# Kernel tuning notes

Hardware: AMD Instinct MI355X
Metric: run time of the kernel (lower is better)

## Reference

```python
import jax, jax.numpy as jnp
import numpy as np


def _unpack_int4(w_i32):
    # w_i32: [N, K//8] int32, 8 signed int4 nibbles per int32 (low nibble first)
    shifts = jnp.arange(8, dtype=jnp.int32) * 4
    nib = (w_i32[:, :, None] >> shifts[None, None, :]) & 0xF  # [N, K//8, 8]
    signed = (nib ^ 8) - 8  # map [0,15] -> [-8,7]
    N = w_i32.shape[0]
    return signed.reshape(N, -1)  # [N, K] int32 in [-8,7]


def setup_inputs() -> dict:
    key = jax.random.key(0)
    k1, k2, k3, k4, k5 = jax.random.split(key, 5)
    M, K, N, G = 4096, 4096, 14336, 128
    qx = jax.random.normal(k1, (M, K), dtype=jnp.float32)
    qxscale = jax.random.uniform(k2, (M, 1), dtype=jnp.float32, minval=0.5, maxval=1.5)
    weight_i4 = jax.random.randint(k3, (N, K // 8), 0, 2147483647, dtype=jnp.int32)
    weight_scale = jax.random.uniform(k4, (N, K // G), dtype=jnp.float32, minval=0.001, maxval=0.02)
    bias = jax.random.normal(k5, (N,), dtype=jnp.float32) * 0.02
    return {"qx": qx, "qxscale": qxscale, "weight_i4": weight_i4,
            "weight_scale": weight_scale, "bias": bias, "group_size": G}


def reference(qx, qxscale, weight_i4, weight_scale, bias, group_size):
    # 1) unpack int32 -> int4  2) per-group dequant  3) matmul  4) scale+bias  5) silu
    iweight = _unpack_int4(weight_i4)  # [N, K]
    N, K = iweight.shape
    deq_w = (iweight.astype(jnp.float32).reshape(N, K // group_size, group_size)
             * weight_scale[:, :, None]).reshape(N, K)  # [N, K]
    y = jnp.einsum('mk,nk->mn', qx, deq_w) * qxscale  # [M, N]
    y = y + bias[None, :]
    return jax.nn.silu(y)
```

## Files before the change

kernel.cpp:

```cpp
#include <hip/hip_runtime.h>
#include <hip/hip_bf16.h>
#include <stdint.h>


#define M_DIM 4096
#define K_DIM 4096
#define N_DIM 14336
#define GSZ   128

typedef __bf16 bf16x8 __attribute__((ext_vector_type(8)));
typedef __bf16 bf16x4 __attribute__((ext_vector_type(4)));
typedef float  f32x4  __attribute__((ext_vector_type(4)));
typedef float  f32x16 __attribute__((ext_vector_type(16)));

#define GLOAD16(g, l) __builtin_amdgcn_global_load_lds( \
    (const __attribute__((address_space(1))) void*)(g), \
    (__attribute__((address_space(3))) void*)(l), 16, 0, 0)

#define WAITVM(N) asm volatile("s_waitcnt vmcnt(" #N ")" ::: "memory")
#define WAITLGKM0() asm volatile("s_waitcnt lgkmcnt(0)" ::: "memory")


__global__ __launch_bounds__(256) void convertA_kernel(
    const float* __restrict__ qx, __bf16* __restrict__ out)
{
    const size_t i = ((size_t)blockIdx.x * 256 + threadIdx.x) * 8;
    const float4 a = *(const float4*)(qx + i);
    const float4 b = *(const float4*)(qx + i + 4);
    bf16x8 v;
    v[0] = (__bf16)a.x; v[1] = (__bf16)a.y; v[2] = (__bf16)a.z; v[3] = (__bf16)a.w;
    v[4] = (__bf16)b.x; v[5] = (__bf16)b.y; v[6] = (__bf16)b.z; v[7] = (__bf16)b.w;
    *(bf16x8*)(out + i) = v;
}

__global__ __launch_bounds__(256) void dequantW_kernel(
    const int* __restrict__ wq, const float* __restrict__ wscale,
    __bf16* __restrict__ out)
{
    const size_t g = (size_t)blockIdx.x * 256 + threadIdx.x;
    const int n  = (int)(g >> 9);
    const int wi = (int)(g & 511);
    const float s = wscale[(size_t)n * (K_DIM / GSZ) + (wi >> 4)];
    const int w = wq[g];
    bf16x8 v;
    #pragma unroll
    for (int j = 0; j < 8; ++j) {
        const int q = ((int)((unsigned)w << (28 - 4 * j))) >> 28;
        v[j] = (__bf16)((float)q * s);
    }
    *(bf16x8*)(out + g * 8) = v;
}


constexpr int BM = 256, BN = 256, BK = 64;
constexpr int NT  = K_DIM / BK;
constexpr int NIT = NT / 2;
constexpr int BUF_BYTES = 65536;

__global__ __launch_bounds__(512, 2) void gemm256_kernel(
    const __bf16* __restrict__ A,
    const __bf16* __restrict__ B,
    const float* __restrict__ qxscale,
    const float* __restrict__ bias,
    float* __restrict__ out)
{
    __shared__ __align__(16) char smem[2 * BUF_BYTES];

    const int t    = threadIdx.x;
    const int lane = t & 63;
    const int wave = t >> 6;
    const int wr   = wave >> 2;
    const int wc   = wave & 3;

    const int bid = blockIdx.x;
    const int cpx = (M_DIM / BM) * (N_DIM / BN) / 8;
    const int wg  = (bid & 7) * cpx + (bid >> 3);
    const int tiles_n = N_DIM / BN;
    const int tm = wg / tiles_n, tn = wg % tiles_n;
    const int m0 = tm * BM, n0 = tn * BN;

    const int srow = t >> 3;
    const int sg16 = (((t & 7) ^ (srow & 7)) << 4);
    const size_t KB = (size_t)K_DIM * 2;
    const char* aS = (const char*)A + (size_t)(m0 + srow) * KB + sg16;
    const char* bS = (const char*)B + (size_t)(n0 + srow) * KB + sg16;
    char* sbase = smem;

    auto STAGE_AQ = [&](int tile, int q) {
        GLOAD16(aS + (size_t)tile * 128 + (size_t)q * 64 * KB,
                sbase + (tile & 1) * BUF_BYTES + q * 8192 + t * 16);
    };
    auto STAGE_BQ = [&](int tile, int q) {
        GLOAD16(bS + (size_t)tile * 128 + (size_t)q * 64 * KB,
                sbase + (tile & 1) * BUF_BYTES + 32768 + q * 8192 + t * 16);
    };

    const int lane31 = lane & 31;
    const int h      = lane >> 5;
    const int swz0   = ((h ^ (lane31 & 7)) << 4);
    const int aB = (wr * 128 + lane31) * 128 + swz0;
    const int bB = 32768 + (wc * 64 + lane31) * 128 + swz0;

    f32x16 acc[4][2] = {};
    bf16x8 af[2][4], bfr[2][4];

    auto DS_A = [&](const char* buf, int mibase) {
        #pragma unroll
        for (int mi = 0; mi < 2; ++mi)
            #pragma unroll
            for (int kk = 0; kk < 4; ++kk)
                af[mi][kk] = *(const bf16x8*)(buf +
                    ((aB + (mibase + mi) * 4096) ^ (kk << 5)));
    };
    auto DS_B = [&](const char* buf, int ni) {
        #pragma unroll
        for (int kk = 0; kk < 4; ++kk)
            bfr[ni][kk] = *(const bf16x8*)(buf +
                ((bB + ni * 4096) ^ (kk << 5)));
    };
    auto MQ = [&](int mib, int ni) {
        #pragma unroll
        for (int kk = 0; kk < 4; ++kk)
            #pragma unroll
            for (int mi = 0; mi < 2; ++mi)
                acc[mib + mi][ni] = __builtin_amdgcn_mfma_f32_32x32x16_bf16(
                    af[mi][kk], bfr[ni][kk], acc[mib + mi][ni], 0, 0, 0);
    };

    #define PH_SYNC() do { __builtin_amdgcn_s_barrier(); WAITLGKM0(); \
        __builtin_amdgcn_sched_barrier(0); __builtin_amdgcn_s_setprio(1); } while (0)
    #define PH_END() do { __builtin_amdgcn_s_setprio(0); \
        __builtin_amdgcn_s_barrier(); } while (0)

    #pragma unroll
    for (int q = 0; q < 4; ++q) STAGE_AQ(0, q);
    #pragma unroll
    for (int q = 0; q < 4; ++q) STAGE_BQ(0, q);
    STAGE_AQ(1, 0); STAGE_AQ(1, 2);
    #pragma unroll
    for (int q = 0; q < 4; ++q) STAGE_BQ(1, q);
    WAITVM(6);
    __builtin_amdgcn_s_barrier();
    __builtin_amdgcn_sched_barrier(0);

    for (int i = 0; i < NIT; ++i) {
        const int t0 = 2 * i, t1 = 2 * i + 1;
        const bool more = (i + 1 < NIT);
        const char* bufE = sbase;
        const char* bufO = sbase + BUF_BYTES;

        DS_A(bufE, 0); DS_B(bufE, 0);
        STAGE_AQ(t1, 1); STAGE_AQ(t1, 3);
        PH_SYNC(); MQ(0, 0); PH_END();

        DS_B(bufE, 1);
        if (more) { STAGE_AQ(t0 + 2, 0); STAGE_AQ(t0 + 2, 2); }
        PH_SYNC(); MQ(0, 1); PH_END();

        DS_A(bufE, 2);
        if (more) { STAGE_BQ(t0 + 2, 0); STAGE_BQ(t0 + 2, 1); }
        PH_SYNC(); MQ(2, 1); PH_END();

        if (more) { STAGE_BQ(t0 + 2, 2); STAGE_BQ(t0 + 2, 3); WAITVM(6); }
        else      { WAITVM(0); }
        __builtin_amdgcn_s_barrier();
        __builtin_amdgcn_sched_barrier(0);
        __builtin_amdgcn_s_setprio(1);
        MQ(2, 0);
        PH_END();

        DS_A(bufO, 0); DS_B(bufO, 0);
        if (more) { STAGE_AQ(t0 + 2, 1); STAGE_AQ(t0 + 2, 3); }
        PH_SYNC(); MQ(0, 0); PH_END();

        DS_B(bufO, 1);
        if (more) { STAGE_AQ(t1 + 2, 0); STAGE_AQ(t1 + 2, 2); }
        PH_SYNC(); MQ(0, 1); PH_END();

        DS_A(bufO, 2);
        if (more) { STAGE_BQ(t1 + 2, 0); STAGE_BQ(t1 + 2, 1); }
        PH_SYNC(); MQ(2, 1); PH_END();

        if (more) { STAGE_BQ(t1 + 2, 2); STAGE_BQ(t1 + 2, 3); WAITVM(6); }
        __builtin_amdgcn_s_barrier();
        __builtin_amdgcn_sched_barrier(0);
        __builtin_amdgcn_s_setprio(1);
        MQ(2, 0);
        PH_END();
    }

    #undef PH_SYNC
    #undef PH_END

    const int c_col = lane31;
    const int hh4   = h * 4;
    float bv[2];
    #pragma unroll
    for (int ni = 0; ni < 2; ++ni)
        bv[ni] = bias[n0 + wc * 64 + ni * 32 + c_col];
    #pragma unroll
    for (int mi = 0; mi < 4; ++mi) {
        #pragma unroll
        for (int rq = 0; rq < 4; ++rq) {
            const int mg = m0 + wr * 128 + mi * 32 + rq * 8 + hh4;
            float qs[4];
            #pragma unroll
            for (int r = 0; r < 4; ++r) qs[r] = qxscale[mg + r];
            #pragma unroll
            for (int ni = 0; ni < 2; ++ni) {
                const int ng = n0 + wc * 64 + ni * 32 + c_col;
                #pragma unroll
                for (int r = 0; r < 4; ++r) {
                    const float y = acc[mi][ni][rq * 4 + r] * qs[r] + bv[ni];
                    out[(size_t)(mg + r) * N_DIM + ng] = y / (1.f + __expf(-y));
                }
            }
        }
    }
}


constexpr int FBM = 128, FBN = 128, FBK = 64;
constexpr int FLDA = 72;

__global__ __launch_bounds__(256) void gateproj_fused_kernel(
    const float* __restrict__ qx, const float* __restrict__ qxscale,
    const int* __restrict__ wq, const float* __restrict__ wscale,
    const float* __restrict__ bias, float* __restrict__ out)
{
    __shared__ __bf16 sA[FBM * FLDA];
    __shared__ __bf16 sB[FBN * FLDA];

    const int tid  = threadIdx.x;
    const int lane = tid & 63;
    const int wave = tid >> 6;
    const int wm = wave >> 1, wn = wave & 1;

    const int bid = blockIdx.x;
    const int cpx = (M_DIM / FBM) * (N_DIM / FBN) / 8;
    const int wg  = (bid & 7) * cpx + (bid >> 3);
    const int tiles_n = N_DIM / FBN;
    const int tm = wg / tiles_n, tn = wg % tiles_n;
    const int m0 = tm * FBM, n0 = tn * FBN;

    const int a_row = tid >> 4;
    const int a_col = (tid & 15) * 4;
    const float* aPtr = qx + (size_t)(m0 + a_row) * K_DIM + a_col;

    const int b_row = tid >> 1;
    const int b_wb  = (tid & 1) * 4;
    const int*   bPtr = wq     + (size_t)(n0 + b_row) * (K_DIM / 8) + b_wb;
    const float* sPtr = wscale + (size_t)(n0 + b_row) * (K_DIM / GSZ);

    float4 aReg[8];
    int    bRegW[4];
    float  bScl;
    f32x4 acc[4][4] = {};

    auto LOAD = [&](int kt) {
        const float* ap = aPtr + kt * FBK;
        #pragma unroll
        for (int i = 0; i < 8; ++i)
            aReg[i] = *(const float4*)(ap + (size_t)i * 16 * K_DIM);
        int4 b = *(const int4*)(bPtr + kt * 8);
        bRegW[0] = b.x; bRegW[1] = b.y; bRegW[2] = b.z; bRegW[3] = b.w;
        bScl = sPtr[kt >> 1];
    };

    auto STORE = [&]() {
        #pragma unroll
        for (int i = 0; i < 8; ++i) {
            bf16x4 v;
            v[0] = (__bf16)aReg[i].x; v[1] = (__bf16)aReg[i].y;
            v[2] = (__bf16)aReg[i].z; v[3] = (__bf16)aReg[i].w;
            *(bf16x4*)&sA[(a_row + i * 16) * FLDA + a_col] = v;
        }
        const int cb = (tid & 1) * 32;
        #pragma unroll
        for (int wi = 0; wi < 4; ++wi) {
            const int w = bRegW[wi];
            bf16x8 o;
            #pragma unroll
            for (int j = 0; j < 8; ++j) {
                const int v = ((int)((unsigned)w << (28 - 4 * j))) >> 28;
                o[j] = (__bf16)((float)v * bScl);
            }
            *(bf16x8*)&sB[b_row * FLDA + cb + wi * 8] = o;
        }
    };

    LOAD(0); STORE(); __syncthreads();

    const int FNT = K_DIM / FBK;
    for (int kt = 0; kt < FNT; ++kt) {
        if (kt + 1 < FNT) LOAD(kt + 1);
        #pragma unroll
        for (int kk = 0; kk < 2; ++kk) {
            bf16x8 af2[4], bfr2[4];
            const int ko = kk * 32 + (lane >> 4) * 8;
            #pragma unroll
            for (int mi = 0; mi < 4; ++mi)
                af2[mi] = *(const bf16x8*)&sA[(wm * 64 + mi * 16 + (lane & 15)) * FLDA + ko];
            #pragma unroll
            for (int ni = 0; ni < 4; ++ni)
                bfr2[ni] = *(const bf16x8*)&sB[(wn * 64 + ni * 16 + (lane & 15)) * FLDA + ko];
            #pragma unroll
            for (int mi = 0; mi < 4; ++mi)
                #pragma unroll
                for (int ni = 0; ni < 4; ++ni)
                    acc[mi][ni] = __builtin_amdgcn_mfma_f32_16x16x32_bf16(
                        af2[mi], bfr2[ni], acc[mi][ni], 0, 0, 0);
        }
        __syncthreads();
        if (kt + 1 < FNT) { STORE(); __syncthreads(); }
    }

    const int c_col = lane & 15;
    const int c_r4  = (lane >> 4) * 4;
    #pragma unroll
    for (int mi = 0; mi < 4; ++mi) {
        const int mg = m0 + wm * 64 + mi * 16 + c_r4;
        float qs[4];
        #pragma unroll
        for (int r = 0; r < 4; ++r) qs[r] = qxscale[mg + r];
        #pragma unroll
        for (int ni = 0; ni < 4; ++ni) {
            const int ng = n0 + wn * 64 + ni * 16 + c_col;
            const float bv = bias[ng];
            #pragma unroll
            for (int r = 0; r < 4; ++r) {
                const float y = acc[mi][ni][r] * qs[r] + bv;
                out[(size_t)(mg + r) * N_DIM + ng] = y / (1.f + __expf(-y));
            }
        }
    }
}


extern "C" void kernel_launch(void* const* d_in, const int* in_sizes, int n_in,
                              void* d_out, int out_size, void* d_ws, size_t ws_size,
                              hipStream_t stream) {
    const float* qx      = (const float*)d_in[0];
    const float* qxscale = (const float*)d_in[1];
    const int*   wq      = (const int*)d_in[2];
    const float* wscale  = (const float*)d_in[3];
    const float* bias    = (const float*)d_in[4];
    float* out = (float*)d_out;

    const size_t needA = (size_t)M_DIM * K_DIM * 2;
    const size_t needW = (size_t)N_DIM * K_DIM * 2;

    if (ws_size >= needA + needW) {
        __bf16* Abf = (__bf16*)d_ws;
        __bf16* Wbf = Abf + (size_t)M_DIM * K_DIM;

        hipLaunchKernelGGL(convertA_kernel, dim3(M_DIM * K_DIM / 8 / 256), dim3(256),
                           0, stream, qx, Abf);
        hipLaunchKernelGGL(dequantW_kernel, dim3(N_DIM * (K_DIM / 8) / 256), dim3(256),
                           0, stream, wq, wscale, Wbf);

        const int grid = (M_DIM / BM) * (N_DIM / BN);
        hipLaunchKernelGGL(gemm256_kernel, dim3(grid), dim3(512), 0, stream,
                           Abf, Wbf, qxscale, bias, out);
    } else {
        const int grid = (M_DIM / FBM) * (N_DIM / FBN);
        hipLaunchKernelGGL(gateproj_fused_kernel, dim3(grid), dim3(256), 0, stream,
                           qx, qxscale, wq, wscale, bias, out);
    }
}
```

Before: 584.1 us.

## Pre-tile A and B into 64x64 blocked layout for contiguous LDS staging

The bf16 conversion and dequant kernels now write A and B in a blocked layout of 64-row by 64-k tiles, arranged k-chunk-major inside each tile. Each global-to-LDS load in the GEMM then reads one contiguous 8 KB block instead of strided rows. This removes the XOR swizzle from the LDS addressing and simplifies the fragment reads. The risk is LDS bank conflicts, since the swizzle is gone, and scattered writes in the producer kernels.

```diff
diff --git a/kernel.cpp b/kernel.cpp
--- a/kernel.cpp
+++ b/kernel.cpp
@@ -25,12 +25,16 @@
     const float* __restrict__ qx, __bf16* __restrict__ out)
 {
     const size_t i = ((size_t)blockIdx.x * 256 + threadIdx.x) * 8;
+    const int row = (int)(i >> 12);
+    const int k   = (int)(i & 4095);
     const float4 a = *(const float4*)(qx + i);
     const float4 b = *(const float4*)(qx + i + 4);
     bf16x8 v;
     v[0] = (__bf16)a.x; v[1] = (__bf16)a.y; v[2] = (__bf16)a.z; v[3] = (__bf16)a.w;
     v[4] = (__bf16)b.x; v[5] = (__bf16)b.y; v[6] = (__bf16)b.z; v[7] = (__bf16)b.w;
-    *(bf16x8*)(out + i) = v;
+    const size_t off = ((((size_t)(row >> 6)) * 64 + (k >> 6)) * 512
+                        + (size_t)((k >> 3) & 7) * 64 + (row & 63)) * 8;
+    *(bf16x8*)(out + off) = v;
 }
 
 __global__ __launch_bounds__(256) void dequantW_kernel(
@@ -48,7 +52,9 @@
         const int q = ((int)((unsigned)w << (28 - 4 * j))) >> 28;
         v[j] = (__bf16)((float)q * s);
     }
-    *(bf16x8*)(out + g * 8) = v;
+    const size_t off = ((((size_t)(n >> 6)) * 64 + (wi >> 3)) * 512
+                        + (size_t)(wi & 7) * 64 + (n & 63)) * 8;
+    *(bf16x8*)(out + off) = v;
 }
 
 
@@ -56,6 +62,7 @@
 constexpr int NT  = K_DIM / BK;
 constexpr int NIT = NT / 2;
 constexpr int BUF_BYTES = 65536;
+constexpr size_t TB = 8192;
 
 __global__ __launch_bounds__(512, 2) void gemm256_kernel(
     const __bf16* __restrict__ A,
@@ -79,44 +86,41 @@
     const int tm = wg / tiles_n, tn = wg % tiles_n;
     const int m0 = tm * BM, n0 = tn * BN;
 
-    const int srow = t >> 3;
-    const int sg16 = (((t & 7) ^ (srow & 7)) << 4);
-    const size_t KB = (size_t)K_DIM * 2;
-    const char* aS = (const char*)A + (size_t)(m0 + srow) * KB + sg16;
-    const char* bS = (const char*)B + (size_t)(n0 + srow) * KB + sg16;
+    const char* aWS = (const char*)A;
+    const char* bWS = (const char*)B;
     char* sbase = smem;
 
     auto STAGE_AQ = [&](int tile, int q) {
-        GLOAD16(aS + (size_t)tile * 128 + (size_t)q * 64 * KB,
+        GLOAD16(aWS + (((size_t)(m0 >> 6) + q) * 64 + tile) * TB + t * 16,
                 sbase + (tile & 1) * BUF_BYTES + q * 8192 + t * 16);
     };
     auto STAGE_BQ = [&](int tile, int q) {
-        GLOAD16(bS + (size_t)tile * 128 + (size_t)q * 64 * KB,
+        GLOAD16(bWS + (((size_t)(n0 >> 6) + q) * 64 + tile) * TB + t * 16,
                 sbase + (tile & 1) * BUF_BYTES + 32768 + q * 8192 + t * 16);
     };
 
     const int lane31 = lane & 31;
     const int h      = lane >> 5;
-    const int swz0   = ((h ^ (lane31 & 7)) << 4);
-    const int aB = (wr * 128 + lane31) * 128 + swz0;
-    const int bB = 32768 + (wc * 64 + lane31) * 128 + swz0;
+    const int aOff = h * 1024 + lane31 * 16;
+    const int bOff = 32768 + wc * 8192 + h * 1024 + lane31 * 16;
 
     f32x16 acc[4][2] = {};
     bf16x8 af[2][4], bfr[2][4];
 
     auto DS_A = [&](const char* buf, int mibase) {
         #pragma unroll
-        for (int mi = 0; mi < 2; ++mi)
+        for (int mi = 0; mi < 2; ++mi) {
+            const int ma = mibase + mi;
+            const int base = (wr * 2 + (ma >> 1)) * 8192 + (ma & 1) * 512 + aOff;
             #pragma unroll
             for (int kk = 0; kk < 4; ++kk)
-                af[mi][kk] = *(const bf16x8*)(buf +
-                    ((aB + (mibase + mi) * 4096) ^ (kk << 5)));
+                af[mi][kk] = *(const bf16x8*)(buf + base + kk * 2048);
+        }
     };
     auto DS_B = [&](const char* buf, int ni) {
         #pragma unroll
         for (int kk = 0; kk < 4; ++kk)
-            bfr[ni][kk] = *(const bf16x8*)(buf +
-                ((bB + ni * 4096) ^ (kk << 5)));
+            bfr[ni][kk] = *(const bf16x8*)(buf + bOff + ni * 512 + kk * 2048);
     };
     auto MQ = [&](int mib, int ni) {
         #pragma unroll
```

New measurement: 625.4 us. 7.1% more time.
